# Performance work log

Measured on AMD Instinct MI355X. Metric: run time of the kernel, lower is better.

## Reference

```python
import jax, jax.numpy as jnp
import numpy as np


def _gcn_conv(h, src, dst, W, b, n):
    # PyG GCNConv: x @ W, then symmetric-normalized aggregation with self-loops
    deg = jax.ops.segment_sum(jnp.ones(src.shape[0], h.dtype), dst, num_segments=n)
    dinv = jax.lax.rsqrt(jnp.maximum(deg, 1.0))  # deg >= 1 because self-loops are included
    norm = dinv[src] * dinv[dst]                 # [E]
    m = (h @ W)[src] * norm[:, None]             # gather + scale
    return jax.ops.segment_sum(m, dst, num_segments=n) + b


def setup_inputs() -> dict:
    key = jax.random.key(0)
    N, E, F, H, L, V = 50000, 800000, 128, 256, 64, 128
    ks = jax.random.split(key, 16)
    s = lambda fan_in: 1.0 / np.sqrt(fan_in)
    return {
        "x": jax.random.randint(ks[0], (N,), 0, V),
        "edge_index": jax.random.randint(ks[1], (2, E), 0, N),
        "eps": jax.random.normal(ks[2], (N, L), jnp.float32),
        "emb": jax.random.normal(ks[3], (V, F), jnp.float32),
        "W1": jax.random.normal(ks[4], (F, H), jnp.float32) * s(F),
        "b1": jnp.zeros((H,), jnp.float32),
        "W2": jax.random.normal(ks[5], (H, H), jnp.float32) * s(H),
        "b2": jnp.zeros((H,), jnp.float32),
        "Wmu": jax.random.normal(ks[6], (H, L), jnp.float32) * s(H),
        "bmu": jnp.zeros((L,), jnp.float32),
        "Wlv": jax.random.normal(ks[7], (H, L), jnp.float32) * s(H),
        "blv": jnp.zeros((L,), jnp.float32),
        "W3": jax.random.normal(ks[8], (L, H), jnp.float32) * s(L),
        "b3": jnp.zeros((H,), jnp.float32),
        "W4": jax.random.normal(ks[9], (H, V), jnp.float32) * s(H),
        "b4": jnp.zeros((V,), jnp.float32),
        "Wcap": jax.random.normal(ks[10], (L, 1), jnp.float32) * s(L),
        "bcap": jnp.zeros((1,), jnp.float32),
    }


def reference(x, edge_index, eps, emb, W1, b1, W2, b2, Wmu, bmu, Wlv, blv, W3, b3, W4, b4, Wcap, bcap):
    n = x.shape[0]
    loops = jnp.arange(n, dtype=edge_index.dtype)
    src = jnp.concatenate([edge_index[0], loops])  # add self-loops once, reuse
    dst = jnp.concatenate([edge_index[1], loops])

    h = emb[x]                                      # [N, F] embedding lookup
    h = jax.nn.relu(_gcn_conv(h, src, dst, W1, b1, n))
    h = jax.nn.relu(_gcn_conv(h, src, dst, W2, b2, n))
    mu = h @ Wmu + bmu
    logvar = h @ Wlv + blv
    z = mu + eps * jnp.exp(0.5 * logvar)            # reparameterize
    recon_x = jax.nn.relu(z @ W3 + b3) @ W4 + b4    # decode
    capitalize = jax.nn.sigmoid(z @ Wcap + bcap)
    return recon_x, capitalize, mu, logvar
```

## Files before the change

kernel.cpp:

```cpp
#include <hip/hip_runtime.h>
#include <math.h>


typedef __attribute__((ext_vector_type(8))) short bf16x8;
typedef __attribute__((ext_vector_type(4))) float f32x4;

__device__ inline unsigned short f2bf(float x) {
    unsigned u = __float_as_uint(x);
    return (unsigned short)((u + 0x7FFFu + ((u >> 16) & 1u)) >> 16);
}
__device__ inline float bf2f(unsigned short h) {
    return __uint_as_float(((unsigned)h) << 16);
}

__global__ __launch_bounds__(256) void k_deg_count(const int* __restrict__ dst,
                                                   int* __restrict__ degint, int E) {
    int e = blockIdx.x * 256 + threadIdx.x;
    if (e < E) atomicAdd(&degint[dst[e]], 1);
}

#define SCAN_BLOCK 1024
__global__ __launch_bounds__(SCAN_BLOCK) void k_scan_local(
        const int* __restrict__ degint, int* __restrict__ row_ptr,
        int* __restrict__ bsum, float* __restrict__ dinv, int N) {
    __shared__ int s[SCAN_BLOCK];
    int gid = blockIdx.x * SCAN_BLOCK + threadIdx.x;
    int d = (gid < N) ? (degint[gid] + 1) : 0;
    if (gid < N) dinv[gid] = rsqrtf((float)d);
    s[threadIdx.x] = d;
    __syncthreads();
    for (int off = 1; off < SCAN_BLOCK; off <<= 1) {
        int t = (threadIdx.x >= off) ? s[threadIdx.x - off] : 0;
        __syncthreads();
        s[threadIdx.x] += t;
        __syncthreads();
    }
    if (gid < N) row_ptr[gid] = s[threadIdx.x] - d;
    if (threadIdx.x == SCAN_BLOCK - 1) bsum[blockIdx.x] = s[SCAN_BLOCK - 1];
}

__global__ void k_scan_bsum(int* __restrict__ bsum, int nb) {
    if (blockIdx.x == 0 && threadIdx.x == 0) {
        int acc = 0;
        for (int i = 0; i < nb; ++i) { int v = bsum[i]; bsum[i] = acc; acc += v; }
    }
}

__global__ __launch_bounds__(256) void k_scan_add(int* __restrict__ row_ptr,
                                                  const int* __restrict__ bsum,
                                                  int N, int T) {
    int gid = blockIdx.x * 256 + threadIdx.x;
    if (gid < N) row_ptr[gid] += bsum[gid / SCAN_BLOCK];
    if (gid == 0) row_ptr[N] = T;
}

__global__ __launch_bounds__(256) void k_fill(
        const int* __restrict__ src, const int* __restrict__ dst,
        const int* __restrict__ x, const float* __restrict__ dinv,
        const int* __restrict__ row_ptr, int* __restrict__ cursor,
        int2* __restrict__ packA, int2* __restrict__ packB, int E, int N) {
    int e = blockIdx.x * 256 + threadIdx.x;
    if (e < E) {
        int s = src[e], d = dst[e];
        float w = dinv[s] * dinv[d];
        int pos = row_ptr[d] + atomicAdd(&cursor[d], 1);
        packA[pos] = make_int2(__float_as_int(w), x[s]);
        packB[pos] = make_int2(__float_as_int(w), s);
    } else if (e < E + N) {
        int i = e - E;
        float di = dinv[i];
        float w = di * di;
        int pos = row_ptr[i] + atomicAdd(&cursor[i], 1);
        packA[pos] = make_int2(__float_as_int(w), x[i]);
        packB[pos] = make_int2(__float_as_int(w), i);
    }
}

__global__ __launch_bounds__(256) void k_cvt_all(
        const float* __restrict__ B0, unsigned short* __restrict__ h0, int K0, int N0,
        const float* __restrict__ B1, unsigned short* __restrict__ h1, int K1, int N1,
        const float* __restrict__ B2, unsigned short* __restrict__ h2, int K2, int N2,
        const float* __restrict__ B3, unsigned short* __restrict__ h3, int K3, int N3,
        const float* __restrict__ B4, unsigned short* __restrict__ h4, int K4, int N4) {
    const float* B; unsigned short* Bh; int K, Ncol;
    switch (blockIdx.y) {
        case 0: B = B0; Bh = h0; K = K0; Ncol = N0; break;
        case 1: B = B1; Bh = h1; K = K1; Ncol = N1; break;
        case 2: B = B2; Bh = h2; K = K2; Ncol = N2; break;
        case 3: B = B3; Bh = h3; K = K3; Ncol = N3; break;
        default: B = B4; Bh = h4; K = K4; Ncol = N4; break;
    }
    int i = blockIdx.x * 256 + threadIdx.x;
    if (i >= K * Ncol) return;
    int k = i / Ncol, n = i - k * Ncol;
    Bh[(long)n * K + k] = f2bf(B[i]);
}

__global__ __launch_bounds__(256) void k_gemm_f32(
        const float* __restrict__ A, const float* __restrict__ B,
        unsigned short* __restrict__ Cb, int M, int K, int Ncol) {
    constexpr int BM = 64, BN = 64, BK = 16;
    __shared__ float As[BK][BM];
    __shared__ float Bs[BK][BN];
    const int tid = threadIdx.x;
    const int tx = tid & 15, ty = tid >> 4;
    const int rowBase = blockIdx.x * BM;
    const int colBase = blockIdx.y * BN;
    const int lr = tid >> 2, lc4 = tid & 3;
    const int br = tid >> 4, bc4 = tid & 15;
    const int arow = rowBase + lr;
    const int K4 = K >> 2, N4 = Ncol >> 2;
    const float4* A4 = (const float4*)A;
    const float4* B4 = (const float4*)B;
    float acc[4][4] = {{0.f}};
    for (int k0 = 0; k0 < K; k0 += BK) {
        float4 av = make_float4(0.f, 0.f, 0.f, 0.f);
        if (arow < M) av = A4[(long)arow * K4 + (k0 >> 2) + lc4];
        As[lc4 * 4 + 0][lr] = av.x;
        As[lc4 * 4 + 1][lr] = av.y;
        As[lc4 * 4 + 2][lr] = av.z;
        As[lc4 * 4 + 3][lr] = av.w;
        float4 bv = B4[(long)(k0 + br) * N4 + (colBase >> 2) + bc4];
        *(float4*)&Bs[br][bc4 * 4] = bv;
        __syncthreads();
#pragma unroll
        for (int k = 0; k < BK; ++k) {
            float4 a4v = *(const float4*)&As[k][ty * 4];
            float4 b4v = *(const float4*)&Bs[k][tx * 4];
            float aa[4] = {a4v.x, a4v.y, a4v.z, a4v.w};
            float bb[4] = {b4v.x, b4v.y, b4v.z, b4v.w};
#pragma unroll
            for (int i = 0; i < 4; ++i)
#pragma unroll
                for (int j = 0; j < 4; ++j)
                    acc[i][j] = fmaf(aa[i], bb[j], acc[i][j]);
        }
        __syncthreads();
    }
#pragma unroll
    for (int i = 0; i < 4; ++i) {
        int row = rowBase + ty * 4 + i;
        if (row < M) {
            ushort4 o;
            o.x = f2bf(acc[i][0]); o.y = f2bf(acc[i][1]);
            o.z = f2bf(acc[i][2]); o.w = f2bf(acc[i][3]);
            *(ushort4*)&Cb[(long)row * Ncol + colBase + tx * 4] = o;
        }
    }
}

template<bool RELU, bool BIAS, bool OUTBF>
__global__ __launch_bounds__(256) void k_gemm_mfma(
        const unsigned short* __restrict__ A, const unsigned short* __restrict__ Bt,
        const float* __restrict__ bias, float* __restrict__ Cf,
        unsigned short* __restrict__ Cb, int M, int K, int Ncol) {
    __shared__ unsigned short Ash[128][40];
    __shared__ unsigned short Bsh[64][40];
    const int tid = threadIdx.x;
    const int lane = tid & 63, w = tid >> 6;
    const int fr = lane & 15, quad = lane >> 4;
    const int wm0 = w * 32;
    const int rowBase = blockIdx.x * 128;
    const int colBase = blockIdx.y * 64;

    const int arow = tid >> 1;
    const int ahalf = (tid & 1) << 4;
    int agrow = rowBase + arow; if (agrow >= M) agrow = M - 1;
    const long abase = (long)agrow * K + ahalf;
    const int brow = tid >> 2;
    const int bseg = (tid & 3) << 3;
    const long bbase = (long)(colBase + brow) * K + bseg;

    f32x4 acc[2][4];
#pragma unroll
    for (int i = 0; i < 2; ++i)
#pragma unroll
        for (int j = 0; j < 4; ++j) acc[i][j] = (f32x4){0.f, 0.f, 0.f, 0.f};

    for (int k0 = 0; k0 < K; k0 += 32) {
        *(bf16x8*)&Ash[arow][ahalf]     = *(const bf16x8*)&A[abase + k0];
        *(bf16x8*)&Ash[arow][ahalf + 8] = *(const bf16x8*)&A[abase + k0 + 8];
        *(bf16x8*)&Bsh[brow][bseg]      = *(const bf16x8*)&Bt[bbase + k0];
        __syncthreads();
        bf16x8 ahf[2], bhf[4];
#pragma unroll
        for (int i = 0; i < 2; ++i)
            ahf[i] = *(const bf16x8*)&Ash[wm0 + i * 16 + fr][quad * 8];
#pragma unroll
        for (int j = 0; j < 4; ++j)
            bhf[j] = *(const bf16x8*)&Bsh[j * 16 + fr][quad * 8];
#pragma unroll
        for (int i = 0; i < 2; ++i)
#pragma unroll
            for (int j = 0; j < 4; ++j)
                acc[i][j] = __builtin_amdgcn_mfma_f32_16x16x32_bf16(
                    ahf[i], bhf[j], acc[i][j], 0, 0, 0);
        __syncthreads();
    }

#pragma unroll
    for (int i = 0; i < 2; ++i) {
        const int rowb = rowBase + wm0 + i * 16 + quad * 4;
#pragma unroll
        for (int j = 0; j < 4; ++j) {
            const int col = colBase + j * 16 + fr;
            const float bv = BIAS ? bias[col] : 0.f;
#pragma unroll
            for (int r = 0; r < 4; ++r) {
                const int row = rowb + r;
                if (row < M) {
                    float v = acc[i][j][r] + bv;
                    if (RELU) v = fmaxf(v, 0.f);
                    const long o = (long)row * Ncol + col;
                    if (OUTBF) Cb[o] = f2bf(v);
                    else       Cf[o] = v;
                }
            }
        }
    }
}

__global__ __launch_bounds__(256) void k_gemm_heads(
        const unsigned short* __restrict__ A, const unsigned short* __restrict__ Bt,
        const float* __restrict__ bmu, const float* __restrict__ blv,
        const float* __restrict__ eps, const float* __restrict__ Wcap,
        const float* __restrict__ bcap, float* __restrict__ mu,
        float* __restrict__ lv, unsigned short* __restrict__ Zh,
        float* __restrict__ cap, int M) {
    constexpr int K = 256;
    __shared__ unsigned short Ash[64][40];
    __shared__ unsigned short Bsh[128][40];
    const int tid = threadIdx.x;
    const int lane = tid & 63, w = tid >> 6;
    const int fr = lane & 15, quad = lane >> 4;
    const int wm0 = w * 16;
    const int rowBase = blockIdx.x * 64;

    const int arow = tid >> 2;
    const int aseg = (tid & 3) << 3;
    int agrow = rowBase + arow; if (agrow >= M) agrow = M - 1;
    const long abase = (long)agrow * K + aseg;
    const int brow = tid >> 1;
    const int bseg = (tid & 1) << 4;
    const long bbase = (long)brow * K + bseg;

    f32x4 acc[8];
#pragma unroll
    for (int j = 0; j < 8; ++j) acc[j] = (f32x4){0.f, 0.f, 0.f, 0.f};

    for (int k0 = 0; k0 < K; k0 += 32) {
        *(bf16x8*)&Ash[arow][aseg] = *(const bf16x8*)&A[abase + k0];
        *(bf16x8*)&Bsh[brow][bseg]     = *(const bf16x8*)&Bt[bbase + k0];
        *(bf16x8*)&Bsh[brow][bseg + 8] = *(const bf16x8*)&Bt[bbase + k0 + 8];
        __syncthreads();
        bf16x8 ahf = *(const bf16x8*)&Ash[wm0 + fr][quad * 8];
#pragma unroll
        for (int j = 0; j < 8; ++j) {
            bf16x8 bhf = *(const bf16x8*)&Bsh[j * 16 + fr][quad * 8];
            acc[j] = __builtin_amdgcn_mfma_f32_16x16x32_bf16(ahf, bhf, acc[j], 0, 0, 0);
        }
        __syncthreads();
    }

    float capacc[4] = {0.f, 0.f, 0.f, 0.f};
#pragma unroll
    for (int j = 0; j < 4; ++j) {
        const int c = j * 16 + fr;
        const float bm = bmu[c], bl = blv[c];
        const float wc = Wcap[c];
#pragma unroll
        for (int r = 0; r < 4; ++r) {
            const int row = rowBase + wm0 + quad * 4 + r;
            if (row < M) {
                const long o = (long)row * 64 + c;
                float mv = acc[j][r] + bm;
                float lvv = acc[j + 4][r] + bl;
                mu[o] = mv;
                lv[o] = lvv;
                float zz = fmaf(eps[o], expf(0.5f * lvv), mv);
                Zh[o] = f2bf(zz);
                capacc[r] = fmaf(zz, wc, capacc[r]);
            }
        }
    }
    const float b0 = bcap[0];
#pragma unroll
    for (int r = 0; r < 4; ++r) {
        float v = capacc[r];
        v += __shfl_xor(v, 1, 64);
        v += __shfl_xor(v, 2, 64);
        v += __shfl_xor(v, 4, 64);
        v += __shfl_xor(v, 8, 64);
        if (fr == 0) {
            const int row = rowBase + wm0 + quad * 4 + r;
            if (row < M) cap[row] = 1.f / (1.f + expf(-(v + b0)));
        }
    }
}

__global__ __launch_bounds__(256) void k_agg_tab(
        const unsigned short* __restrict__ tab, const int* __restrict__ row_ptr,
        const int2* __restrict__ packA, const float* __restrict__ bias,
        unsigned short* __restrict__ h1, int N) {
    const int wave = threadIdx.x >> 6;
    const int lane = threadIdx.x & 63;
    const int node = blockIdx.x * 4 + wave;
    if (node >= N) return;
    const ushort4* t4 = (const ushort4*)tab;
    float ax = 0.f, ay = 0.f, az = 0.f, aw = 0.f;
    const int beg = row_ptr[node], end = row_ptr[node + 1];
    int e = beg;
    for (; e + 4 <= end; e += 4) {
        int2 p0 = packA[e], p1 = packA[e + 1], p2 = packA[e + 2], p3 = packA[e + 3];
        ushort4 v0 = t4[(long)p0.y * 64 + lane];
        ushort4 v1 = t4[(long)p1.y * 64 + lane];
        ushort4 v2 = t4[(long)p2.y * 64 + lane];
        ushort4 v3 = t4[(long)p3.y * 64 + lane];
        float w0 = __int_as_float(p0.x), w1 = __int_as_float(p1.x);
        float w2 = __int_as_float(p2.x), w3 = __int_as_float(p3.x);
        ax = fmaf(bf2f(v0.x), w0, ax); ay = fmaf(bf2f(v0.y), w0, ay);
        az = fmaf(bf2f(v0.z), w0, az); aw = fmaf(bf2f(v0.w), w0, aw);
        ax = fmaf(bf2f(v1.x), w1, ax); ay = fmaf(bf2f(v1.y), w1, ay);
        az = fmaf(bf2f(v1.z), w1, az); aw = fmaf(bf2f(v1.w), w1, aw);
        ax = fmaf(bf2f(v2.x), w2, ax); ay = fmaf(bf2f(v2.y), w2, ay);
        az = fmaf(bf2f(v2.z), w2, az); aw = fmaf(bf2f(v2.w), w2, aw);
        ax = fmaf(bf2f(v3.x), w3, ax); ay = fmaf(bf2f(v3.y), w3, ay);
        az = fmaf(bf2f(v3.z), w3, az); aw = fmaf(bf2f(v3.w), w3, aw);
    }
    for (; e < end; ++e) {
        int2 p = packA[e];
        float w0 = __int_as_float(p.x);
        ushort4 v = t4[(long)p.y * 64 + lane];
        ax = fmaf(bf2f(v.x), w0, ax); ay = fmaf(bf2f(v.y), w0, ay);
        az = fmaf(bf2f(v.z), w0, az); aw = fmaf(bf2f(v.w), w0, aw);
    }
    float4 b = ((const float4*)bias)[lane];
    ax = fmaxf(ax + b.x, 0.f); ay = fmaxf(ay + b.y, 0.f);
    az = fmaxf(az + b.z, 0.f); aw = fmaxf(aw + b.w, 0.f);
    ushort4 o;
    o.x = f2bf(ax); o.y = f2bf(ay); o.z = f2bf(az); o.w = f2bf(aw);
    ((ushort4*)h1)[(long)node * 64 + lane] = o;
}

__global__ __launch_bounds__(256) void k_agg_nb(
        const unsigned short* __restrict__ h1, const int* __restrict__ row_ptr,
        const int2* __restrict__ packB, unsigned short* __restrict__ Ob, int N) {
    const int wave = threadIdx.x >> 6;
    const int lane = threadIdx.x & 63;
    const int node = blockIdx.x * 4 + wave;
    if (node >= N) return;
    const ushort4* h4 = (const ushort4*)h1;
    float ax = 0.f, ay = 0.f, az = 0.f, aw = 0.f;
    const int beg = row_ptr[node], end = row_ptr[node + 1];
    int e = beg;
    for (; e + 4 <= end; e += 4) {
        int2 p0 = packB[e], p1 = packB[e + 1], p2 = packB[e + 2], p3 = packB[e + 3];
        ushort4 v0 = h4[(long)p0.y * 64 + lane];
        ushort4 v1 = h4[(long)p1.y * 64 + lane];
        ushort4 v2 = h4[(long)p2.y * 64 + lane];
        ushort4 v3 = h4[(long)p3.y * 64 + lane];
        float w0 = __int_as_float(p0.x), w1 = __int_as_float(p1.x);
        float w2 = __int_as_float(p2.x), w3 = __int_as_float(p3.x);
        ax = fmaf(bf2f(v0.x), w0, ax); ay = fmaf(bf2f(v0.y), w0, ay);
        az = fmaf(bf2f(v0.z), w0, az); aw = fmaf(bf2f(v0.w), w0, aw);
        ax = fmaf(bf2f(v1.x), w1, ax); ay = fmaf(bf2f(v1.y), w1, ay);
        az = fmaf(bf2f(v1.z), w1, az); aw = fmaf(bf2f(v1.w), w1, aw);
        ax = fmaf(bf2f(v2.x), w2, ax); ay = fmaf(bf2f(v2.y), w2, ay);
        az = fmaf(bf2f(v2.z), w2, az); aw = fmaf(bf2f(v2.w), w2, aw);
        ax = fmaf(bf2f(v3.x), w3, ax); ay = fmaf(bf2f(v3.y), w3, ay);
        az = fmaf(bf2f(v3.z), w3, az); aw = fmaf(bf2f(v3.w), w3, aw);
    }
    for (; e < end; ++e) {
        int2 p = packB[e];
        float w0 = __int_as_float(p.x);
        ushort4 v = h4[(long)p.y * 64 + lane];
        ax = fmaf(bf2f(v.x), w0, ax); ay = fmaf(bf2f(v.y), w0, ay);
        az = fmaf(bf2f(v.z), w0, az); aw = fmaf(bf2f(v.w), w0, aw);
    }
    ushort4 o;
    o.x = f2bf(ax); o.y = f2bf(ay); o.z = f2bf(az); o.w = f2bf(aw);
    ((ushort4*)Ob)[(long)node * 64 + lane] = o;
}

extern "C" void kernel_launch(void* const* d_in, const int* in_sizes, int n_in,
                              void* d_out, int out_size, void* d_ws, size_t ws_size,
                              hipStream_t stream) {
    const int*   x    = (const int*)d_in[0];
    const int*   ei   = (const int*)d_in[1];
    const float* eps  = (const float*)d_in[2];
    const float* emb  = (const float*)d_in[3];
    const float* W1   = (const float*)d_in[4];
    const float* b1   = (const float*)d_in[5];
    const float* W2   = (const float*)d_in[6];
    const float* b2   = (const float*)d_in[7];
    const float* Wmu  = (const float*)d_in[8];
    const float* bmu  = (const float*)d_in[9];
    const float* Wlv  = (const float*)d_in[10];
    const float* blv  = (const float*)d_in[11];
    const float* W3   = (const float*)d_in[12];
    const float* b3   = (const float*)d_in[13];
    const float* W4   = (const float*)d_in[14];
    const float* b4   = (const float*)d_in[15];
    const float* Wcap = (const float*)d_in[16];
    const float* bcap = (const float*)d_in[17];

    const int N = in_sizes[0];
    const int E = in_sizes[1] / 2;
    const int H = in_sizes[5];
    const int L = in_sizes[9];
    const int V = in_sizes[15];
    const int F = in_sizes[4] / H;
    const int T = E + N;

    const int* src = ei;
    const int* dst = ei + E;

    char* w = (char*)d_ws;
    unsigned short* h1b  = (unsigned short*)w; w += (size_t)N * H * 2;
    unsigned short* a2b  = (unsigned short*)w; w += (size_t)N * H * 2;
    unsigned short* h2b  = (unsigned short*)w; w += (size_t)N * H * 2;
    unsigned short* zh   = (unsigned short*)w; w += (size_t)N * L * 2;
    int*   degint = (int*)w;   w += (size_t)N * 4;
    int*   rowp   = (int*)w;   w += (size_t)(N + 1) * 4;
    int*   cursor = (int*)w;   w += (size_t)N * 4;
    float* dinv   = (float*)w; w += (size_t)N * 4;
    int*   bsum   = (int*)w;   w += 256 * 4;
    int2*  packA  = (int2*)w;  w += (size_t)T * 8;
    int2*  packB  = (int2*)w;  w += (size_t)T * 8;
    unsigned short* tabH = (unsigned short*)w; w += (size_t)V * H * 2;
    unsigned short* W2t  = (unsigned short*)w; w += (size_t)H * H * 2;
    unsigned short* Wml  = (unsigned short*)w; w += (size_t)H * 2 * L * 2;
    unsigned short* W3t  = (unsigned short*)w; w += (size_t)L * H * 2;
    unsigned short* W4t  = (unsigned short*)w; w += (size_t)H * V * 2;

    unsigned short* tb = a2b;

    float* outp    = (float*)d_out;
    float* recon   = outp;
    float* cap     = outp + (size_t)N * V;
    float* mu      = outp + (size_t)N * V + N;
    float* logvar  = mu + (size_t)N * L;

    const int nN  = (N + 255) / 256;
    const int nE  = (E + 255) / 256;
    const int nT  = (T + 255) / 256;
    const int nSc = (N + SCAN_BLOCK - 1) / SCAN_BLOCK;
    const int gM128 = (N + 127) / 128;
    const int gM64  = (N + 63) / 64;

    hipMemsetAsync(degint, 0, (size_t)N * 4, stream);
    hipMemsetAsync(cursor, 0, (size_t)N * 4, stream);
    k_deg_count<<<nE, 256, 0, stream>>>(dst, degint, E);
    k_scan_local<<<nSc, SCAN_BLOCK, 0, stream>>>(degint, rowp, bsum, dinv, N);
    k_scan_bsum<<<1, 64, 0, stream>>>(bsum, nSc);
    k_scan_add<<<nN, 256, 0, stream>>>(rowp, bsum, N, T);
    k_fill<<<nT, 256, 0, stream>>>(src, dst, x, dinv, rowp, cursor,
                                   packA, packB, E, N);

    k_cvt_all<<<dim3((H * H + 255) / 256, 5), 256, 0, stream>>>(
        W2, W2t, H, H,
        Wmu, Wml, H, L,
        Wlv, Wml + (size_t)L * H, H, L,
        W3, W3t, L, H,
        W4, W4t, H, V);

    k_gemm_f32<<<dim3(V / 64, H / 64), 256, 0, stream>>>(emb, W1, tabH, V, F, H);
    k_agg_tab<<<(N + 3) / 4, 256, 0, stream>>>(tabH, rowp, packA, b1, h1b, N);

    k_agg_nb<<<(N + 3) / 4, 256, 0, stream>>>(h1b, rowp, packB, a2b, N);
    k_gemm_mfma<true, true, true><<<dim3(gM128, H / 64), 256, 0, stream>>>(
        a2b, W2t, b2, nullptr, h2b, N, H, H);

    k_gemm_heads<<<gM64, 256, 0, stream>>>(
        h2b, Wml, bmu, blv, eps, Wcap, bcap, mu, logvar, zh, cap, N);

    k_gemm_mfma<true, true, true><<<dim3(gM128, H / 64), 256, 0, stream>>>(
        zh, W3t, b3, nullptr, tb, N, L, H);
    k_gemm_mfma<false, true, false><<<dim3(gM128, V / 64), 256, 0, stream>>>(
        tb, W4t, b4, recon, nullptr, N, H, V);
}
```

Before: 427.8 us.

## Merge CSR scan into one kernel and pack edge records into int4

Replaces the three-kernel block scan with a single 1024-thread kernel in which each thread serially scans a chunk of degrees. The two memsets become one by placing cursor next to degint. The two int2 edge arrays become one int4 array, so k_fill writes once per edge, and each fill thread now handles four edges. The aggregation kernels read 16-byte records instead of 8, which raises index-stream traffic, and the single-block scan runs serially over about 49 entries per thread.

```diff
diff --git a/kernel.cpp b/kernel.cpp
--- a/kernel.cpp
+++ b/kernel.cpp
@@ -19,60 +19,54 @@
     if (e < E) atomicAdd(&degint[dst[e]], 1);
 }
 
-#define SCAN_BLOCK 1024
-__global__ __launch_bounds__(SCAN_BLOCK) void k_scan_local(
+__global__ __launch_bounds__(1024) void k_scan_one(
         const int* __restrict__ degint, int* __restrict__ row_ptr,
-        int* __restrict__ bsum, float* __restrict__ dinv, int N) {
-    __shared__ int s[SCAN_BLOCK];
-    int gid = blockIdx.x * SCAN_BLOCK + threadIdx.x;
-    int d = (gid < N) ? (degint[gid] + 1) : 0;
-    if (gid < N) dinv[gid] = rsqrtf((float)d);
-    s[threadIdx.x] = d;
+        float* __restrict__ dinv, int N, int T) {
+    __shared__ int s[1024];
+    const int t = threadIdx.x;
+    const int CH = (N + 1023) >> 10;
+    const int lo = t * CH;
+    const int hi = (lo + CH < N) ? lo + CH : N;
+    int sum = 0;
+    for (int i = lo; i < hi; ++i) sum += degint[i] + 1;
+    s[t] = sum;
     __syncthreads();
-    for (int off = 1; off < SCAN_BLOCK; off <<= 1) {
-        int t = (threadIdx.x >= off) ? s[threadIdx.x - off] : 0;
-        __syncthreads();
-        s[threadIdx.x] += t;
-        __syncthreads();
-    }
-    if (gid < N) row_ptr[gid] = s[threadIdx.x] - d;
-    if (threadIdx.x == SCAN_BLOCK - 1) bsum[blockIdx.x] = s[SCAN_BLOCK - 1];
-}
-
-__global__ void k_scan_bsum(int* __restrict__ bsum, int nb) {
-    if (blockIdx.x == 0 && threadIdx.x == 0) {
-        int acc = 0;
-        for (int i = 0; i < nb; ++i) { int v = bsum[i]; bsum[i] = acc; acc += v; }
-    }
-}
-
-__global__ __launch_bounds__(256) void k_scan_add(int* __restrict__ row_ptr,
-                                                  const int* __restrict__ bsum,
-                                                  int N, int T) {
-    int gid = blockIdx.x * 256 + threadIdx.x;
-    if (gid < N) row_ptr[gid] += bsum[gid / SCAN_BLOCK];
-    if (gid == 0) row_ptr[N] = T;
+    for (int off = 1; off < 1024; off <<= 1) {
+        int v = (t >= off) ? s[t - off] : 0;
+        __syncthreads();
+        s[t] += v;
+        __syncthreads();
+    }
+    int base = s[t] - sum;
+    for (int i = lo; i < hi; ++i) {
+        int d = degint[i] + 1;
+        row_ptr[i] = base;
+        dinv[i] = rsqrtf((float)d);
+        base += d;
+    }
+    if (t == 0) row_ptr[N] = T;
 }
 
 __global__ __launch_bounds__(256) void k_fill(
         const int* __restrict__ src, const int* __restrict__ dst,
         const int* __restrict__ x, const float* __restrict__ dinv,
         const int* __restrict__ row_ptr, int* __restrict__ cursor,
-        int2* __restrict__ packA, int2* __restrict__ packB, int E, int N) {
-    int e = blockIdx.x * 256 + threadIdx.x;
-    if (e < E) {
-        int s = src[e], d = dst[e];
-        float w = dinv[s] * dinv[d];
-        int pos = row_ptr[d] + atomicAdd(&cursor[d], 1);
-        packA[pos] = make_int2(__float_as_int(w), x[s]);
-        packB[pos] = make_int2(__float_as_int(w), s);
-    } else if (e < E + N) {
-        int i = e - E;
-        float di = dinv[i];
-        float w = di * di;
-        int pos = row_ptr[i] + atomicAdd(&cursor[i], 1);
-        packA[pos] = make_int2(__float_as_int(w), x[i]);
-        packB[pos] = make_int2(__float_as_int(w), i);
+        int4* __restrict__ pack, int E, int N) {
+    const int base = (blockIdx.x * 256 + threadIdx.x) * 4;
+#pragma unroll
+    for (int j = 0; j < 4; ++j) {
+        int e = base + j;
+        if (e < E) {
+            int s = src[e], d = dst[e];
+            float w = dinv[s] * dinv[d];
+            int pos = row_ptr[d] + atomicAdd(&cursor[d], 1);
+            pack[pos] = make_int4(__float_as_int(w), x[s], s, 0);
+        } else if (e < E + N) {
+            int i = e - E;
+            float di = dinv[i];
+            int pos = row_ptr[i] + atomicAdd(&cursor[i], 1);
+            pack[pos] = make_int4(__float_as_int(di * di), x[i], i, 0);
+        }
     }
 }
 
@@ -300,7 +294,7 @@
 
 __global__ __launch_bounds__(256) void k_agg_tab(
         const unsigned short* __restrict__ tab, const int* __restrict__ row_ptr,
-        const int2* __restrict__ packA, const float* __restrict__ bias,
+        const int4* __restrict__ pack, const float* __restrict__ bias,
         unsigned short* __restrict__ h1, int N) {
     const int wave = threadIdx.x >> 6;
     const int lane = threadIdx.x & 63;
@@ -311,7 +305,7 @@
     const int beg = row_ptr[node], end = row_ptr[node + 1];
     int e = beg;
     for (; e + 4 <= end; e += 4) {
-        int2 p0 = packA[e], p1 = packA[e + 1], p2 = packA[e + 2], p3 = packA[e + 3];
+        int4 p0 = pack[e], p1 = pack[e + 1], p2 = pack[e + 2], p3 = pack[e + 3];
         ushort4 v0 = t4[(long)p0.y * 64 + lane];
         ushort4 v1 = t4[(long)p1.y * 64 + lane];
         ushort4 v2 = t4[(long)p2.y * 64 + lane];
@@ -328,7 +322,7 @@
         az = fmaf(bf2f(v3.z), w3, az); aw = fmaf(bf2f(v3.w), w3, aw);
     }
     for (; e < end; ++e) {
-        int2 p = packA[e];
+        int4 p = pack[e];
         float w0 = __int_as_float(p.x);
         ushort4 v = t4[(long)p.y * 64 + lane];
         ax = fmaf(bf2f(v.x), w0, ax); ay = fmaf(bf2f(v.y), w0, ay);
@@ -344,7 +338,7 @@
 
 __global__ __launch_bounds__(256) void k_agg_nb(
         const unsigned short* __restrict__ h1, const int* __restrict__ row_ptr,
-        const int2* __restrict__ packB, unsigned short* __restrict__ Ob, int N) {
+        const int4* __restrict__ pack, unsigned short* __restrict__ Ob, int N) {
     const int wave = threadIdx.x >> 6;
     const int lane = threadIdx.x & 63;
     const int node = blockIdx.x * 4 + wave;
@@ -354,11 +348,11 @@
     const int beg = row_ptr[node], end = row_ptr[node + 1];
     int e = beg;
     for (; e + 4 <= end; e += 4) {
-        int2 p0 = packB[e], p1 = packB[e + 1], p2 = packB[e + 2], p3 = packB[e + 3];
-        ushort4 v0 = h4[(long)p0.y * 64 + lane];
-        ushort4 v1 = h4[(long)p1.y * 64 + lane];
-        ushort4 v2 = h4[(long)p2.y * 64 + lane];
-        ushort4 v3 = h4[(long)p3.y * 64 + lane];
+        int4 p0 = pack[e], p1 = pack[e + 1], p2 = pack[e + 2], p3 = pack[e + 3];
+        ushort4 v0 = h4[(long)p0.z * 64 + lane];
+        ushort4 v1 = h4[(long)p1.z * 64 + lane];
+        ushort4 v2 = h4[(long)p2.z * 64 + lane];
+        ushort4 v3 = h4[(long)p3.z * 64 + lane];
         float w0 = __int_as_float(p0.x), w1 = __int_as_float(p1.x);
         float w2 = __int_as_float(p2.x), w3 = __int_as_float(p3.x);
         ax = fmaf(bf2f(v0.x), w0, ax); ay = fmaf(bf2f(v0.y), w0, ay);
@@ -368,12 +362,12 @@
         ax = fmaf(bf2f(v2.x), w2, ax); ay = fmaf(bf2f(v2.y), w2, ay);
         az = fmaf(bf2f(v2.z), w2, az); aw = fmaf(bf2f(v2.w), w2, aw);
         ax = fmaf(bf2f(v3.x), w3, ax); ay = fmaf(bf2f(v3.y), w3, ay);
-        az = fmaf(bf2f(v3.z), w3, az); aw = fmaf(bf2f(v3.w), w3, aw);
+        az = fmaf(bf2f(v3.z), w3, aw == aw ? az : az), aw = fmaf(bf2f(v3.w), w3, aw);
     }
     for (; e < end; ++e) {
-        int2 p = packB[e];
+        int4 p = pack[e];
         float w0 = __int_as_float(p.x);
-        ushort4 v = h4[(long)p.y * 64 + lane];
+        ushort4 v = h4[(long)p.z * 64 + lane];
         ax = fmaf(bf2f(v.x), w0, ax); ay = fmaf(bf2f(v.y), w0, ay);
         az = fmaf(bf2f(v.z), w0, az); aw = fmaf(bf2f(v.w), w0, aw);
     }
@@ -421,12 +415,10 @@
     unsigned short* h2b  = (unsigned short*)w; w += (size_t)N * H * 2;
     unsigned short* zh   = (unsigned short*)w; w += (size_t)N * L * 2;
     int*   degint = (int*)w;   w += (size_t)N * 4;
+    int*   cursor = (int*)w;   w += (size_t)N * 4;
     int*   rowp   = (int*)w;   w += (size_t)(N + 1) * 4;
-    int*   cursor = (int*)w;   w += (size_t)N * 4;
     float* dinv   = (float*)w; w += (size_t)N * 4;
-    int*   bsum   = (int*)w;   w += 256 * 4;
-    int2*  packA  = (int2*)w;  w += (size_t)T * 8;
-    int2*  packB  = (int2*)w;  w += (size_t)T * 8;
+    int4*  pack   = (int4*)w;  w += (size_t)T * 16;
     unsigned short* tabH = (unsigned short*)w; w += (size_t)V * H * 2;
     unsigned short* W2t  = (unsigned short*)w; w += (size_t)H * H * 2;
     unsigned short* Wml  = (unsigned short*)w; w += (size_t)H * 2 * L * 2;
@@ -441,21 +433,15 @@
     float* mu      = outp + (size_t)N * V + N;
     float* logvar  = mu + (size_t)N * L;
 
-    const int nN  = (N + 255) / 256;
     const int nE  = (E + 255) / 256;
-    const int nT  = (T + 255) / 256;
-    const int nSc = (N + SCAN_BLOCK - 1) / SCAN_BLOCK;
+    const int nT4 = (T + 1023) / 1024;
     const int gM128 = (N + 127) / 128;
     const int gM64  = (N + 63) / 64;
 
-    hipMemsetAsync(degint, 0, (size_t)N * 4, stream);
-    hipMemsetAsync(cursor, 0, (size_t)N * 4, stream);
+    hipMemsetAsync(degint, 0, (size_t)N * 8, stream);
     k_deg_count<<<nE, 256, 0, stream>>>(dst, degint, E);
-    k_scan_local<<<nSc, SCAN_BLOCK, 0, stream>>>(degint, rowp, bsum, dinv, N);
-    k_scan_bsum<<<1, 64, 0, stream>>>(bsum, nSc);
-    k_scan_add<<<nN, 256, 0, stream>>>(rowp, bsum, N, T);
-    k_fill<<<nT, 256, 0, stream>>>(src, dst, x, dinv, rowp, cursor,
-                                   packA, packB, E, N);
+    k_scan_one<<<1, 1024, 0, stream>>>(degint, rowp, dinv, N, T);
+    k_fill<<<nT4, 256, 0, stream>>>(src, dst, x, dinv, rowp, cursor, pack, E, N);
 
     k_cvt_all<<<dim3((H * H + 255) / 256, 5), 256, 0, stream>>>(
         W2, W2t, H, H,
@@ -465,9 +451,9 @@
         W4, W4t, H, V);
 
     k_gemm_f32<<<dim3(V / 64, H / 64), 256, 0, stream>>>(emb, W1, tabH, V, F, H);
-    k_agg_tab<<<(N + 3) / 4, 256, 0, stream>>>(tabH, rowp, packA, b1, h1b, N);
-
-    k_agg_nb<<<(N + 3) / 4, 256, 0, stream>>>(h1b, rowp, packB, a2b, N);
+    k_agg_tab<<<(N + 3) / 4, 256, 0, stream>>>(tabH, rowp, pack, b1, h1b, N);
+
+    k_agg_nb<<<(N + 3) / 4, 256, 0, stream>>>(h1b, rowp, pack, a2b, N);
     k_gemm_mfma<true, true, true><<<dim3(gM128, H / 64), 256, 0, stream>>>(
         a2b, W2t, b2, nullptr, h2b, N, H, H);
 
```

New measurement: 515.9 us. 1.21x slower.
